# Kernel tuning notes

Hardware: AMD Instinct MI355X
Metric: run time of the kernel (lower is better)

## Reference

```python
import jax, jax.numpy as jnp
import numpy as np
import math

B, D, C = 256, 512, 100000
SCALE = 64.0
MARGIN = 0.5
ALPHA = 1.2
SIGMA = 2.0
THRESH = math.cos(math.pi - MARGIN)
MM = math.sin(math.pi - MARGIN) * MARGIN


def _l2_normalize(x, axis=-1, eps=1e-12):
    n = jnp.linalg.norm(x, axis=axis, keepdims=True)
    return x / jnp.maximum(n, eps)


def setup_inputs() -> dict:
    key = jax.random.key(0)
    k1, k2, k3 = jax.random.split(key, 3)
    inp = jax.random.normal(k1, (B, D), dtype=jnp.float32)
    label = jax.random.randint(k2, (B,), 0, C, dtype=jnp.int64)
    stdv = 1.0 / math.sqrt(D)
    weight = jax.random.uniform(k3, (C, D), dtype=jnp.float32, minval=-stdv, maxval=stdv)
    return {"input": inp, "label": label, "weight": weight}


def reference(input, label, weight):
    # cosine similarity: [B, C]
    cos = _l2_normalize(input) @ _l2_normalize(weight).T
    rows = jnp.arange(cos.shape[0])
    cos_lb = cos[rows, label]  # [B]
    # angular margin on the target logit, with the standard arcface fallback
    a_lb = jnp.where(
        cos_lb > THRESH,
        jnp.cos(jnp.arccos(jnp.clip(cos_lb, -1.0, 1.0)) + MARGIN),
        cos_lb - MM,
    )  # [B]
    # gaussian reweighting of negatives around the margined target logit (detached)
    t_scale = jax.lax.stop_gradient(
        ALPHA * jnp.exp(-jnp.square(cos - a_lb[:, None]) / SIGMA)
    )  # [B, C]
    onehot = jax.nn.one_hot(label, cos.shape[1], dtype=cos.dtype)  # [B, C]
    logits = SCALE * (
        onehot * a_lb[:, None] + (1.0 - onehot) * (t_scale * cos + t_scale - 1.0)
    )
    return logits
```

## Files before the change

kernel.cpp:

```cpp
#include <hip/hip_runtime.h>
#include <hip/hip_bf16.h>
#include <math.h>

#define B_ 256
#define D_ 512
#define C_ 100000

#define SCALE_  64.0f
#define ALPHA_  1.2f
#define THRESH_ (-0.8775825618903728f)
#define MM_     (0.23971276930210156f)
#define COSM_   (0.8775825618903728f)
#define SINM_   (0.4794255386042030f)

typedef __bf16 bf16x8 __attribute__((ext_vector_type(8)));
typedef __bf16 bf16x4 __attribute__((ext_vector_type(4)));
typedef float  f32x4  __attribute__((ext_vector_type(4)));

__global__ void prep_kernel(const float* __restrict__ inp,
                            const int* __restrict__ lab_raw,
                            const float* __restrict__ weight,
                            __bf16* __restrict__ xnf,
                            float* __restrict__ a_lb,
                            int* __restrict__ lab32) {
    const int b = blockIdx.x;
    const int l = threadIdx.x;

    const bool is64 = (lab_raw[1] == 0) & (lab_raw[3] == 0) & (lab_raw[5] == 0) &
                      (lab_raw[7] == 0) & (lab_raw[9] == 0) & (lab_raw[11] == 0) &
                      (lab_raw[13] == 0) & (lab_raw[15] == 0);
    const int lab = is64 ? lab_raw[2 * b] : lab_raw[b];

    const float* ip = inp + b * D_ + l * 8;
    f32x4 v0 = *(const f32x4*)ip;
    f32x4 v1 = *(const f32x4*)(ip + 4);
    float ss = v0.x * v0.x + v0.y * v0.y + v0.z * v0.z + v0.w * v0.w +
               v1.x * v1.x + v1.y * v1.y + v1.z * v1.z + v1.w * v1.w;
#pragma unroll
    for (int m = 1; m < 64; m <<= 1) ss += __shfl_xor(ss, m);
    const float ninv = 1.0f / fmaxf(sqrtf(ss), 1e-12f);

    float xf[8] = {v0.x * ninv, v0.y * ninv, v0.z * ninv, v0.w * ninv,
                   v1.x * ninv, v1.y * ninv, v1.z * ninv, v1.w * ninv};
    bf16x8 xv;
#pragma unroll
    for (int i = 0; i < 8; ++i) xv[i] = (__bf16)xf[i];

    const int tile_idx = (b >> 4) * 16 + (l >> 2);
    const int lf = (b & 15) + ((l & 3) << 4);
    *(bf16x8*)((char*)xnf + tile_idx * 1024 + lf * 16) = xv;

    const float* wp = weight + (size_t)lab * D_ + l * 8;
    f32x4 w0 = *(const f32x4*)wp;
    f32x4 w1 = *(const f32x4*)(wp + 4);
    float wss = w0.x * w0.x + w0.y * w0.y + w0.z * w0.z + w0.w * w0.w +
                w1.x * w1.x + w1.y * w1.y + w1.z * w1.z + w1.w * w1.w;
    float dp = xf[0] * w0.x + xf[1] * w0.y + xf[2] * w0.z + xf[3] * w0.w +
               xf[4] * w1.x + xf[5] * w1.y + xf[6] * w1.z + xf[7] * w1.w;
#pragma unroll
    for (int m = 1; m < 64; m <<= 1) {
        wss += __shfl_xor(wss, m);
        dp  += __shfl_xor(dp, m);
    }
    if (l == 0) {
        const float cos_lb = dp / fmaxf(sqrtf(wss), 1e-12f);
        const float ccl = fminf(fmaxf(cos_lb, -1.0f), 1.0f);
        const float s = sqrtf(fmaxf(0.0f, 1.0f - ccl * ccl));
        const float a1 = ccl * COSM_ - s * SINM_;
        a_lb[b] = (cos_lb > THRESH_) ? a1 : (cos_lb - MM_);
        lab32[b] = lab;
    }
}

#define BN 64
#define BK 64

__global__ __launch_bounds__(256, 3)
void gemm_kernel(const __bf16* __restrict__ xnf,
                 const float* __restrict__ weight,
                 const float* __restrict__ a_lb,
                 const int* __restrict__ lab32,
                 float* __restrict__ out) {
    __shared__ __align__(16) char wT[BN * BK * 2];
    __shared__ float wssq[BN];

    const int tid  = threadIdx.x;
    const int lane = tid & 63;
    const int wm   = tid >> 6;
    const int n0   = blockIdx.x * BN;

    f32x4 acc[4][4] = {};
    float wss = 0.0f;

    const int wrow = tid >> 2;
    const int wc   = (tid & 3) * 16;
    int grow = n0 + wrow;
    grow = (grow < C_) ? grow : (C_ - 1);
    const float* wbase = weight + (size_t)grow * D_ + wc;

    f32x4 wpre[4];
#pragma unroll
    for (int i = 0; i < 4; ++i) wpre[i] = *(const f32x4*)(wbase + i * 4);

    for (int kt = 0; kt < D_ / BK; ++kt) {
        if (kt) __syncthreads();
        bf16x8 h0, h1;
#pragma unroll
        for (int i = 0; i < 4; ++i) {
            f32x4 v = wpre[i];
            wss += v.x * v.x + v.y * v.y + v.z * v.z + v.w * v.w;
            if (i < 2) {
                h0[i * 4 + 0] = (__bf16)v.x; h0[i * 4 + 1] = (__bf16)v.y;
                h0[i * 4 + 2] = (__bf16)v.z; h0[i * 4 + 3] = (__bf16)v.w;
            } else {
                h1[(i - 2) * 4 + 0] = (__bf16)v.x; h1[(i - 2) * 4 + 1] = (__bf16)v.y;
                h1[(i - 2) * 4 + 2] = (__bf16)v.z; h1[(i - 2) * 4 + 3] = (__bf16)v.w;
            }
        }
        {
            int off0 = wrow * (BK * 2) + wc * 2;
            int off1 = off0 + 16;
            off0 ^= (wrow & 7) << 4;
            off1 ^= (wrow & 7) << 4;
            *(bf16x8*)(wT + off0) = h0;
            *(bf16x8*)(wT + off1) = h1;
        }
        __syncthreads();

        if (kt < D_ / BK - 1) {
            const float* p = wbase + (kt + 1) * BK;
#pragma unroll
            for (int i = 0; i < 4; ++i) wpre[i] = *(const f32x4*)(p + i * 4);
        }

        bf16x8 af[2][4];
#pragma unroll
        for (int ks = 0; ks < 2; ++ks)
#pragma unroll
            for (int m = 0; m < 4; ++m) {
                const int tile = (wm * 4 + m) * 16 + kt * 2 + ks;
                af[ks][m] = *(const bf16x8*)((const char*)xnf + tile * 1024 + lane * 16);
            }

#pragma unroll
        for (int ks = 0; ks < 2; ++ks) {
            bf16x8 bfr[4];
#pragma unroll
            for (int n = 0; n < 4; ++n) {
                const int row = n * 16 + (lane & 15);
                int off = row * (BK * 2) + ks * 64 + (lane >> 4) * 16;
                off ^= (row & 7) << 4;
                bfr[n] = *(const bf16x8*)(wT + off);
            }
#pragma unroll
            for (int m = 0; m < 4; ++m)
#pragma unroll
                for (int n = 0; n < 4; ++n)
                    acc[m][n] = __builtin_amdgcn_mfma_f32_16x16x32_bf16(
                        af[ks][m], bfr[n], acc[m][n], 0, 0, 0);
        }
    }

    {
        float s = wss;
        s += __shfl_xor(s, 1);
        s += __shfl_xor(s, 2);
        if ((tid & 3) == 0) wssq[wrow] = s;
    }
    __syncthreads();

    float al_r[16];
    int   lb_r[16];
    const int rb0 = wm * 64 + ((lane >> 4) << 2);
#pragma unroll
    for (int m = 0; m < 4; ++m)
#pragma unroll
        for (int j = 0; j < 4; ++j) {
            const int b = rb0 + m * 16 + j;
            al_r[m * 4 + j] = a_lb[b];
            lb_r[m * 4 + j] = lab32[b];
        }

#pragma unroll
    for (int n = 0; n < 4; ++n) {
        const int ln = n * 16 + (lane & 15);
        const int c = n0 + ln;
        const float winv = 1.0f / fmaxf(sqrtf(wssq[ln]), 1e-12f);
        const bool ok = (c < C_);
#pragma unroll
        for (int m = 0; m < 4; ++m)
#pragma unroll
            for (int j = 0; j < 4; ++j) {
                const int b = rb0 + m * 16 + j;
                const float al = al_r[m * 4 + j];
                const float cosv = acc[m][n][j] * winv;
                const float d = cosv - al;
                const float t = ALPHA_ * __expf(-0.5f * d * d);
                const float o = (c == lb_r[m * 4 + j]) ? al : (t * cosv + t - 1.0f);
                if (ok) out[(size_t)b * C_ + c] = SCALE_ * o;
            }
    }
}

extern "C" void kernel_launch(void* const* d_in, const int* in_sizes, int n_in,
                              void* d_out, int out_size, void* d_ws, size_t ws_size,
                              hipStream_t stream) {
    const float* inp = (const float*)d_in[0];
    const int*   lab = (const int*)d_in[1];
    const float* w   = (const float*)d_in[2];
    float* out = (float*)d_out;

    char* ws = (char*)d_ws;
    __bf16* xnf  = (__bf16*)ws;
    float*  a_lb = (float*)(ws + 262144);
    int*    l32  = (int*)(ws + 262144 + 1024);

    prep_kernel<<<B_, 64, 0, stream>>>(inp, lab, w, xnf, a_lb, l32);
    gemm_kernel<<<(C_ + BN - 1) / BN, 256, 0, stream>>>(xnf, w, a_lb, l32, out);
}
```

Before: 88.88 us.

## Stage full-K weight panel in LDS with narrower N tile and register double buffering

The GEMM kernel now uses 32 classes per block and loads each block's whole 32x512 weight panel into LDS in one pass, replacing the 8-step K loop that had a barrier on every step. Row norms are computed with wave-level reductions during the load. The K loop then double-buffers A and B fragments in registers with no further barriers. The grid grows to 3125 blocks, and bounds checks are removed because C divides evenly by 32. In exchange, LDS use per block rises to 32 KB, and each block reads the whole input tile for half as much output.

```diff
diff --git a/kernel.cpp b/kernel.cpp
--- a/kernel.cpp
+++ b/kernel.cpp
@@ -72,8 +72,7 @@
     }
 }
 
-#define BN 64
-#define BK 64
+#define BN 32
 
 __global__ __launch_bounds__(256, 3)
 void gemm_kernel(const __bf16* __restrict__ xnf,
@@ -81,97 +80,90 @@
                  const float* __restrict__ a_lb,
                  const int* __restrict__ lab32,
                  float* __restrict__ out) {
-    __shared__ __align__(16) char wT[BN * BK * 2];
+    __shared__ __align__(16) char wT[BN * D_ * 2];
     __shared__ float wssq[BN];
 
     const int tid  = threadIdx.x;
     const int lane = tid & 63;
-    const int wm   = tid >> 6;
+    const int w    = tid >> 6;
     const int n0   = blockIdx.x * BN;
 
-    f32x4 acc[4][4] = {};
-    float wss = 0.0f;
-
-    const int wrow = tid >> 2;
-    const int wc   = (tid & 3) * 16;
-    int grow = n0 + wrow;
-    grow = (grow < C_) ? grow : (C_ - 1);
-    const float* wbase = weight + (size_t)grow * D_ + wc;
-
-    f32x4 wpre[4];
-#pragma unroll
-    for (int i = 0; i < 4; ++i) wpre[i] = *(const f32x4*)(wbase + i * 4);
-
-    for (int kt = 0; kt < D_ / BK; ++kt) {
-        if (kt) __syncthreads();
-        bf16x8 h0, h1;
-#pragma unroll
-        for (int i = 0; i < 4; ++i) {
-            f32x4 v = wpre[i];
-            wss += v.x * v.x + v.y * v.y + v.z * v.z + v.w * v.w;
-            if (i < 2) {
-                h0[i * 4 + 0] = (__bf16)v.x; h0[i * 4 + 1] = (__bf16)v.y;
-                h0[i * 4 + 2] = (__bf16)v.z; h0[i * 4 + 3] = (__bf16)v.w;
-            } else {
-                h1[(i - 2) * 4 + 0] = (__bf16)v.x; h1[(i - 2) * 4 + 1] = (__bf16)v.y;
-                h1[(i - 2) * 4 + 2] = (__bf16)v.z; h1[(i - 2) * 4 + 3] = (__bf16)v.w;
+    f32x4 acc[4][2] = {};
+
+    const float* wpanel = weight + (size_t)(n0 + w * 8) * D_;
+
+    f32x4 wva[8], wvb[8];
+#pragma unroll
+    for (int i = 0; i < 8; ++i)
+        wva[i] = *(const f32x4*)(wpanel + (i >> 1) * D_ + (i & 1) * 256 + lane * 4);
+#pragma unroll
+    for (int i = 0; i < 8; ++i)
+        wvb[i] = *(const f32x4*)(wpanel + ((i + 8) >> 1) * D_ + (i & 1) * 256 + lane * 4);
+
+    bf16x8 af[2][4];
+#pragma unroll
+    for (int m = 0; m < 4; ++m)
+        af[0][m] = *(const bf16x8*)((const char*)xnf + ((w * 4 + m) * 16 + 0) * 1024 + lane * 16);
+
+#pragma unroll
+    for (int c = 0; c < 2; ++c) {
+        float ss = 0.0f;
+#pragma unroll
+        for (int i = 0; i < 8; ++i) {
+            f32x4 v = (c == 0) ? wva[i] : wvb[i];
+            ss += v.x * v.x + v.y * v.y + v.z * v.z + v.w * v.w;
+            bf16x4 h;
+            h[0] = (__bf16)v.x; h[1] = (__bf16)v.y;
+            h[2] = (__bf16)v.z; h[3] = (__bf16)v.w;
+            const int row = w * 8 + c * 4 + (i >> 1);
+            int off = row * (D_ * 2) + (i & 1) * 512 + lane * 8;
+            off ^= (row & 7) << 4;
+            *(bf16x4*)(wT + off) = h;
+            if (i & 1) {
+#pragma unroll
+                for (int msk = 1; msk < 64; msk <<= 1) ss += __shfl_xor(ss, msk);
+                if (lane == 0) wssq[row] = ss;
+                ss = 0.0f;
             }
         }
-        {
-            int off0 = wrow * (BK * 2) + wc * 2;
-            int off1 = off0 + 16;
-            off0 ^= (wrow & 7) << 4;
-            off1 ^= (wrow & 7) << 4;
-            *(bf16x8*)(wT + off0) = h0;
-            *(bf16x8*)(wT + off1) = h1;
+    }
+    __syncthreads();
+
+    bf16x8 bfr[2][2];
+#pragma unroll
+    for (int n = 0; n < 2; ++n) {
+        const int row = n * 16 + (lane & 15);
+        int off = row * (D_ * 2) + 0 * 64 + (lane >> 4) * 16;
+        off ^= (row & 7) << 4;
+        bfr[0][n] = *(const bf16x8*)(wT + off);
+    }
+
+    for (int ks = 0; ks < 16; ++ks) {
+        const int cur = ks & 1, nxt = cur ^ 1;
+        if (ks < 15) {
+#pragma unroll
+            for (int m = 0; m < 4; ++m)
+                af[nxt][m] = *(const bf16x8*)((const char*)xnf +
+                             ((w * 4 + m) * 16 + ks + 1) * 1024 + lane * 16);
+#pragma unroll
+            for (int n = 0; n < 2; ++n) {
+                const int row = n * 16 + (lane & 15);
+                int off = row * (D_ * 2) + (ks + 1) * 64 + (lane >> 4) * 16;
+                off ^= (row & 7) << 4;
+                bfr[nxt][n] = *(const bf16x8*)(wT + off);
+            }
         }
-        __syncthreads();
-
-        if (kt < D_ / BK - 1) {
-            const float* p = wbase + (kt + 1) * BK;
-#pragma unroll
-            for (int i = 0; i < 4; ++i) wpre[i] = *(const f32x4*)(p + i * 4);
-        }
-
-        bf16x8 af[2][4];
-#pragma unroll
-        for (int ks = 0; ks < 2; ++ks)
-#pragma unroll
-            for (int m = 0; m < 4; ++m) {
-                const int tile = (wm * 4 + m) * 16 + kt * 2 + ks;
-                af[ks][m] = *(const bf16x8*)((const char*)xnf + tile * 1024 + lane * 16);
-            }
-
-#pragma unroll
-        for (int ks = 0; ks < 2; ++ks) {
-            bf16x8 bfr[4];
-#pragma unroll
-            for (int n = 0; n < 4; ++n) {
-                const int row = n * 16 + (lane & 15);
-                int off = row * (BK * 2) + ks * 64 + (lane >> 4) * 16;
-                off ^= (row & 7) << 4;
-                bfr[n] = *(const bf16x8*)(wT + off);
-            }
-#pragma unroll
-            for (int m = 0; m < 4; ++m)
-#pragma unroll
-                for (int n = 0; n < 4; ++n)
-                    acc[m][n] = __builtin_amdgcn_mfma_f32_16x16x32_bf16(
-                        af[ks][m], bfr[n], acc[m][n], 0, 0, 0);
-        }
-    }
-
-    {
-        float s = wss;
-        s += __shfl_xor(s, 1);
-        s += __shfl_xor(s, 2);
-        if ((tid & 3) == 0) wssq[wrow] = s;
-    }
-    __syncthreads();
+#pragma unroll
+        for (int m = 0; m < 4; ++m)
+#pragma unroll
+            for (int n = 0; n < 2; ++n)
+                acc[m][n] = __builtin_amdgcn_mfma_f32_16x16x32_bf16(
+                    af[cur][m], bfr[cur][n], acc[m][n], 0, 0, 0);
+    }
 
     float al_r[16];
     int   lb_r[16];
-    const int rb0 = wm * 64 + ((lane >> 4) << 2);
+    const int rb0 = w * 64 + ((lane >> 4) << 2);
 #pragma unroll
     for (int m = 0; m < 4; ++m)
 #pragma unroll
@@ -182,11 +174,10 @@
         }
 
 #pragma unroll
-    for (int n = 0; n < 4; ++n) {
+    for (int n = 0; n < 2; ++n) {
         const int ln = n * 16 + (lane & 15);
         const int c = n0 + ln;
         const float winv = 1.0f / fmaxf(sqrtf(wssq[ln]), 1e-12f);
-        const bool ok = (c < C_);
 #pragma unroll
         for (int m = 0; m < 4; ++m)
 #pragma unroll
@@ -197,7 +188,7 @@
                 const float d = cosv - al;
                 const float t = ALPHA_ * __expf(-0.5f * d * d);
                 const float o = (c == lb_r[m * 4 + j]) ? al : (t * cosv + t - 1.0f);
-                if (ok) out[(size_t)b * C_ + c] = SCALE_ * o;
+                out[(size_t)b * C_ + c] = SCALE_ * o;
             }
     }
 }
@@ -216,5 +207,5 @@
     int*    l32  = (int*)(ws + 262144 + 1024);
 
     prep_kernel<<<B_, 64, 0, stream>>>(inp, lab, w, xnf, a_lb, l32);
-    gemm_kernel<<<(C_ + BN - 1) / BN, 256, 0, stream>>>(xnf, w, a_lb, l32, out);
+    gemm_kernel<<<C_ / BN, 256, 0, stream>>>(xnf, w, a_lb, l32, out);
 }
```

Measured after the change: 89.59 us. No clear change (+0.8%).
